# Optimization experiments

Hardware: AMD Instinct MI355X
Metric: run time of the kernel (lower is better)

Reference implementation:

```python
import jax, jax.numpy as jnp
import numpy as np

RESOLUTION = 256
THRESHOLD = 0.01
N_SAMPLES = 16_000_000


def setup_inputs() -> dict:
    key = jax.random.key(0)
    k1, k2 = jax.random.split(key)
    # torch.rand(n_samples, 3): uniform in [0,1) before AABB scaling
    points = jax.random.uniform(k1, (N_SAMPLES, 3), dtype=jnp.float32)
    # densities produced by the NeRF model; uniform [0,1) stand-in
    densities = jax.random.uniform(k2, (N_SAMPLES,), dtype=jnp.float32)
    return {"points": points, "densities": densities}


def reference(points, densities):
    aabb_min = jnp.array([-1.0, -1.0, -1.0], dtype=jnp.float32)
    aabb_max = jnp.array([1.0, 1.0, 1.0], dtype=jnp.float32)
    extent = aabb_max - aabb_min
    # scale unit-cube samples into the AABB (as update_grid does)
    pts = aabb_min + points * extent  # [N, 3]
    # voxel coords: ((p - min) / extent * R).long(), clamped to [0, R-1]
    coords = ((pts - aabb_min) / extent * RESOLUTION).astype(jnp.int32)
    coords = jnp.clip(coords, 0, RESOLUTION - 1)  # [N, 3]
    # loop writes 1.0 only where density > threshold; max over mask is equivalent
    occ = (densities > THRESHOLD).astype(jnp.float32)  # [N]
    grid = jnp.zeros((RESOLUTION, RESOLUTION, RESOLUTION), dtype=jnp.float32)
    grid = grid.at[coords[:, 0], coords[:, 1], coords[:, 2]].max(occ)
    return grid
```

## Files before the change

kernel.cpp:

```cpp
#include <hip/hip_runtime.h>

#define RES 256
#define THRESH 0.01f
#define GRID_VOX (RES * RES * RES)
#define NB 256
#define CHUNK_REC 8192
#define K1_BLOCKS 2048
#define QPT 8

typedef float vf4 __attribute__((ext_vector_type(4)));
typedef unsigned int u32;
typedef unsigned short u16;
typedef u32 vu4 __attribute__((ext_vector_type(4)));

__device__ __forceinline__ int voxel_coord(float p) {
    float a = -1.0f + p * 2.0f;
    float c = ((a + 1.0f) * 0.5f) * 256.0f;
    int v = (int)c;
    v = v < 0 ? 0 : v;
    v = v > (RES - 1) ? (RES - 1) : v;
    return v;
}

__global__ __launch_bounds__(256) void k1_bin256(const vf4* __restrict__ pts4,
                                                 const vf4* __restrict__ dens4,
                                                 u32* __restrict__ regions32,
                                                 u32* __restrict__ meta,
                                                 int n4) {
    __shared__ u32 s_cnt[NB];
    __shared__ u32 s_off[NB];
    __shared__ u32 s_buf[CHUNK_REC];

    const int tid  = threadIdx.x;
    const int lane = tid & 63;
    const int wid  = tid >> 6;
    const int T    = gridDim.x * blockDim.x;
    const int t0   = blockIdx.x * blockDim.x + tid;

    s_cnt[tid] = 0;
    __syncthreads();

    u32 rec[QPT * 4], rnk[QPT * 4], vbits = 0;

    #pragma unroll
    for (int h = 0; h < 2; ++h) {
        vf4 P[4][3], D[4];
        u32 qm = 0;
        #pragma unroll
        for (int s2 = 0; s2 < 4; ++s2) {
            int q = t0 + (h * 4 + s2) * T;
            if (q < n4) {
                qm |= 1u << s2;
                P[s2][0] = __builtin_nontemporal_load(&pts4[3 * q + 0]);
                P[s2][1] = __builtin_nontemporal_load(&pts4[3 * q + 1]);
                P[s2][2] = __builtin_nontemporal_load(&pts4[3 * q + 2]);
                D[s2]    = __builtin_nontemporal_load(&dens4[q]);
            }
        }
        #pragma unroll
        for (int s2 = 0; s2 < 4; ++s2) {
            if (!((qm >> s2) & 1u)) continue;
            float px[4] = {P[s2][0].x, P[s2][0].w, P[s2][1].z, P[s2][2].y};
            float py[4] = {P[s2][0].y, P[s2][1].x, P[s2][1].w, P[s2][2].z};
            float pz[4] = {P[s2][0].z, P[s2][1].y, P[s2][2].x, P[s2][2].w};
            float dd[4] = {D[s2].x, D[s2].y, D[s2].z, D[s2].w};
            #pragma unroll
            for (int k = 0; k < 4; ++k) {
                int kk = (h * 4 + s2) * 4 + k;
                u32 vox = ((u32)voxel_coord(px[k]) << 16) |
                          ((u32)voxel_coord(py[k]) << 8)  |
                           (u32)voxel_coord(pz[k]);
                rec[kk] = vox;
                if (dd[k] > THRESH) {
                    vbits |= 1u << kk;
                    rnk[kk] = atomicAdd(&s_cnt[vox >> 16], 1u);
                }
            }
        }
    }
    __syncthreads();

    if (wid == 0) {
        u32 c0 = s_cnt[4 * lane + 0], c1 = s_cnt[4 * lane + 1];
        u32 c2 = s_cnt[4 * lane + 2], c3 = s_cnt[4 * lane + 3];
        u32 w = c0 + c1 + c2 + c3;
        u32 x = w;
        #pragma unroll
        for (int dlt = 1; dlt < 64; dlt <<= 1) {
            u32 v = __shfl_up(x, dlt, 64);
            if (lane >= dlt) x += v;
        }
        u32 base = x - w;
        s_off[4 * lane + 0] = base;
        s_off[4 * lane + 1] = base + c0;
        s_off[4 * lane + 2] = base + c0 + c1;
        s_off[4 * lane + 3] = base + c0 + c1 + c2;
    }
    __syncthreads();

    const u32 c = blockIdx.x;

    meta[(size_t)c * NB + tid] = s_off[tid] | (s_cnt[tid] << 16);

    #pragma unroll
    for (int kk = 0; kk < QPT * 4; ++kk)
        if ((vbits >> kk) & 1u) {
            u32 b = rec[kk] >> 16;
            s_buf[s_off[b] + rnk[kk]] = rec[kk];
        }
    __syncthreads();

    u32 total = s_off[NB - 1] + s_cnt[NB - 1];
    u32 nw = (total + 1) >> 1;
    u32* reg = regions32 + (size_t)c * (CHUNK_REC / 2);
    for (u32 idx = tid; idx < nw; idx += 256u) {
        u32 lo = s_buf[2 * idx] & 0xFFFFu;
        u32 hi = s_buf[2 * idx + 1] & 0xFFFFu;
        reg[idx] = lo | (hi << 16);
    }
}

__global__ __launch_bounds__(1024) void k2_plane(const u16* __restrict__ regions16,
                                                 const u32* __restrict__ meta,
                                                 vf4* __restrict__ out4,
                                                 int nchunk) {
    extern __shared__ unsigned char plane[];
    const int ix  = blockIdx.x;
    const int tid = threadIdx.x;

    uint4* p16 = (uint4*)plane;
    #pragma unroll
    for (int j = 0; j < 4; ++j)
        p16[tid + j * 1024] = make_uint4(0u, 0u, 0u, 0u);
    __syncthreads();

    for (int c = tid; c < nchunk; c += 1024) {
        u32 m = meta[(size_t)c * NB + ix];
        u32 off = m & 0xFFFFu;
        u32 cnt = m >> 16;
        const u16* run = regions16 + (size_t)c * CHUNK_REC + off;
        for (u32 j = 0; j < cnt; ++j)
            plane[run[j]] = (unsigned char)1;
    }
    __syncthreads();

    const u32* pw = (const u32*)plane;
    vf4* dst = out4 + ((size_t)ix << 14);
    #pragma unroll
    for (int j = 0; j < 16; ++j) {
        int i = tid + j * 1024;
        u32 w = pw[i];
        vf4 f;
        f.x = (w & 0x000000FFu) ? 1.0f : 0.0f;
        f.y = (w & 0x0000FF00u) ? 1.0f : 0.0f;
        f.z = (w & 0x00FF0000u) ? 1.0f : 0.0f;
        f.w = (w & 0xFF000000u) ? 1.0f : 0.0f;
        __builtin_nontemporal_store(f, &dst[i]);
    }
}

__global__ void occ_scatter_bytes(const vf4* __restrict__ pts4,
                                  const vf4* __restrict__ dens4,
                                  unsigned char* __restrict__ bgrid, int n4) {
    int t = blockIdx.x * blockDim.x + threadIdx.x;
    int stride = gridDim.x * blockDim.x;
    for (int i = t; i < n4; i += stride) {
        vf4 p0 = __builtin_nontemporal_load(&pts4[3 * i + 0]);
        vf4 p1 = __builtin_nontemporal_load(&pts4[3 * i + 1]);
        vf4 p2 = __builtin_nontemporal_load(&pts4[3 * i + 2]);
        vf4 d  = __builtin_nontemporal_load(&dens4[i]);
        float px[4] = {p0.x, p0.w, p1.z, p2.y};
        float py[4] = {p0.y, p1.x, p1.w, p2.z};
        float pz[4] = {p0.z, p1.y, p2.x, p2.w};
        float dd[4] = {d.x, d.y, d.z, d.w};
        #pragma unroll
        for (int k = 0; k < 4; ++k) {
            if (dd[k] > THRESH) {
                int ix = voxel_coord(px[k]);
                int iy = voxel_coord(py[k]);
                int iz = voxel_coord(pz[k]);
                bgrid[((ix << 8) | iy) * RES + iz] = (unsigned char)1;
            }
        }
    }
}

__global__ void occ_expand(const uint4* __restrict__ bgrid16,
                           float4* __restrict__ grid4) {
    int i = blockIdx.x * blockDim.x + threadIdx.x;
    uint4 w = bgrid16[i];
    unsigned int ws[4] = {w.x, w.y, w.z, w.w};
    #pragma unroll
    for (int q = 0; q < 4; ++q) {
        unsigned int v = ws[q];
        float4 f;
        f.x = (v & 0x000000FFu) ? 1.0f : 0.0f;
        f.y = (v & 0x0000FF00u) ? 1.0f : 0.0f;
        f.z = (v & 0x00FF0000u) ? 1.0f : 0.0f;
        f.w = (v & 0xFF000000u) ? 1.0f : 0.0f;
        grid4[i * 4 + q] = f;
    }
}

__global__ void occ_scatter_float(const float4* __restrict__ pts4,
                                  const float4* __restrict__ dens4,
                                  float* __restrict__ grid, int n4) {
    int t = blockIdx.x * blockDim.x + threadIdx.x;
    int stride = gridDim.x * blockDim.x;
    for (int i = t; i < n4; i += stride) {
        float4 p0 = pts4[3 * i + 0];
        float4 p1 = pts4[3 * i + 1];
        float4 p2 = pts4[3 * i + 2];
        float4 d  = dens4[i];
        float px[4] = {p0.x, p0.w, p1.z, p2.y};
        float py[4] = {p0.y, p1.x, p1.w, p2.z};
        float pz[4] = {p0.z, p1.y, p2.x, p2.w};
        float dd[4] = {d.x, d.y, d.z, d.w};
        #pragma unroll
        for (int k = 0; k < 4; ++k) {
            if (dd[k] > THRESH) {
                int ix = voxel_coord(px[k]);
                int iy = voxel_coord(py[k]);
                int iz = voxel_coord(pz[k]);
                grid[((ix * RES) + iy) * RES + iz] = 1.0f;
            }
        }
    }
}

extern "C" void kernel_launch(void* const* d_in, const int* in_sizes, int n_in,
                              void* d_out, int out_size, void* d_ws, size_t ws_size,
                              hipStream_t stream) {
    const float* points    = (const float*)d_in[0];
    const float* densities = (const float*)d_in[1];
    float* grid = (float*)d_out;

    int n  = in_sizes[1];
    int n4 = n / 4;

    const int nchunk = K1_BLOCKS;

    size_t metaSize = (size_t)nchunk * NB * sizeof(u32);
    size_t need = metaSize + (size_t)nchunk * CHUNK_REC * sizeof(u16);

    bool covered = (size_t)K1_BLOCKS * 256 * QPT >= (size_t)n4;

    if (ws_size >= need && covered) {
        u32* meta      = (u32*)d_ws;
        u32* regions32 = (u32*)((char*)d_ws + metaSize);
        const u16* regions16 = (const u16*)regions32;

        k1_bin256<<<K1_BLOCKS, 256, 0, stream>>>(
            (const vf4*)points, (const vf4*)densities, regions32, meta, n4);

        k2_plane<<<NB, 1024, 65536, stream>>>(regions16, meta, (vf4*)grid, nchunk);
    } else if (ws_size >= (size_t)GRID_VOX) {
        unsigned char* bgrid = (unsigned char*)d_ws;
        (void)hipMemsetAsync(d_ws, 0, (size_t)GRID_VOX, stream);
        occ_scatter_bytes<<<2048, 256, 0, stream>>>(
            (const vf4*)points, (const vf4*)densities, bgrid, n4);
        occ_expand<<<GRID_VOX / (16 * 256), 256, 0, stream>>>(
            (const uint4*)bgrid, (float4*)grid);
    } else {
        (void)hipMemsetAsync(d_out, 0, (size_t)out_size * sizeof(float), stream);
        occ_scatter_float<<<2048, 256, 0, stream>>>(
            (const float4*)points, (const float4*)densities, grid, n4);
    }
}
```

Baseline: 107.4 us.

## Bin into 512 half-plane buckets and software-pipeline loads in binning kernel

The binning kernel now uses 512 buckets (half x-planes) instead of 256, so the plane kernel runs 512 blocks with 32KB LDS each, raising occupancy and parallelism in the scatter/expand stage. Loads are double-buffered in pairs with sched barriers to overlap memory with compute, and register rank arrays are replaced by a second atomic pass on per-bucket cursors. The LDS staging buffer is halved by writing 16-bit records directly, removing the repacking step. The cost is doubled metadata size, extra LDS atomics, and more meta reads in the plane kernel.

```diff
diff --git a/kernel.cpp b/kernel.cpp
--- a/kernel.cpp
+++ b/kernel.cpp
@@ -3,10 +3,10 @@
 #define RES 256
 #define THRESH 0.01f
 #define GRID_VOX (RES * RES * RES)
-#define NB 256
+#define NBUCK 512
 #define CHUNK_REC 8192
 #define K1_BLOCKS 2048
-#define QPT 8
+#define PAIRS 4
 
 typedef float vf4 __attribute__((ext_vector_type(4)));
 typedef unsigned int u32;
@@ -22,14 +22,16 @@
     return v;
 }
 
-__global__ __launch_bounds__(256) void k1_bin256(const vf4* __restrict__ pts4,
+__global__ __launch_bounds__(256) void k1_bin512(const vf4* __restrict__ pts4,
                                                  const vf4* __restrict__ dens4,
                                                  u32* __restrict__ regions32,
                                                  u32* __restrict__ meta,
                                                  int n4) {
-    __shared__ u32 s_cnt[NB];
-    __shared__ u32 s_off[NB];
-    __shared__ u32 s_buf[CHUNK_REC];
+    __shared__ u32 s_cnt[NBUCK];
+    __shared__ u32 s_off[NBUCK];
+    __shared__ u32 s_pos[NBUCK];
+    __shared__ u32 s_buf32[CHUNK_REC / 2];
+    u16* s_buf16 = (u16*)s_buf32;
 
     const int tid  = threadIdx.x;
     const int lane = tid & 63;
@@ -38,42 +40,64 @@
     const int t0   = blockIdx.x * blockDim.x + tid;
 
     s_cnt[tid] = 0;
-    __syncthreads();
-
-    u32 rec[QPT * 4], rnk[QPT * 4], vbits = 0;
-
-    #pragma unroll
-    for (int h = 0; h < 2; ++h) {
-        vf4 P[4][3], D[4];
-        u32 qm = 0;
-        #pragma unroll
-        for (int s2 = 0; s2 < 4; ++s2) {
-            int q = t0 + (h * 4 + s2) * T;
-            if (q < n4) {
-                qm |= 1u << s2;
-                P[s2][0] = __builtin_nontemporal_load(&pts4[3 * q + 0]);
-                P[s2][1] = __builtin_nontemporal_load(&pts4[3 * q + 1]);
-                P[s2][2] = __builtin_nontemporal_load(&pts4[3 * q + 2]);
-                D[s2]    = __builtin_nontemporal_load(&dens4[q]);
-            }
-        }
-        #pragma unroll
-        for (int s2 = 0; s2 < 4; ++s2) {
-            if (!((qm >> s2) & 1u)) continue;
-            float px[4] = {P[s2][0].x, P[s2][0].w, P[s2][1].z, P[s2][2].y};
-            float py[4] = {P[s2][0].y, P[s2][1].x, P[s2][1].w, P[s2][2].z};
-            float pz[4] = {P[s2][0].z, P[s2][1].y, P[s2][2].x, P[s2][2].w};
-            float dd[4] = {D[s2].x, D[s2].y, D[s2].z, D[s2].w};
+    s_cnt[tid + 256] = 0;
+    __syncthreads();
+
+    u32 rec[PAIRS * 8];
+    u32 vbits = 0;
+
+    vf4 P[2][2][3], D[2][2];
+    u32 qm[2];
+
+    qm[0] = 0;
+    #pragma unroll
+    for (int j = 0; j < 2; ++j) {
+        int q = t0 + j * T;
+        if (q < n4) {
+            qm[0] |= 1u << j;
+            P[0][j][0] = __builtin_nontemporal_load(&pts4[3 * q + 0]);
+            P[0][j][1] = __builtin_nontemporal_load(&pts4[3 * q + 1]);
+            P[0][j][2] = __builtin_nontemporal_load(&pts4[3 * q + 2]);
+            D[0][j]    = __builtin_nontemporal_load(&dens4[q]);
+        }
+    }
+    __builtin_amdgcn_sched_barrier(0);
+
+    #pragma unroll
+    for (int p = 0; p < PAIRS; ++p) {
+        const int cur = p & 1, nxt = cur ^ 1;
+        if (p < PAIRS - 1) {
+            qm[nxt] = 0;
+            #pragma unroll
+            for (int j = 0; j < 2; ++j) {
+                int q = t0 + ((p + 1) * 2 + j) * T;
+                if (q < n4) {
+                    qm[nxt] |= 1u << j;
+                    P[nxt][j][0] = __builtin_nontemporal_load(&pts4[3 * q + 0]);
+                    P[nxt][j][1] = __builtin_nontemporal_load(&pts4[3 * q + 1]);
+                    P[nxt][j][2] = __builtin_nontemporal_load(&pts4[3 * q + 2]);
+                    D[nxt][j]    = __builtin_nontemporal_load(&dens4[q]);
+                }
+            }
+            __builtin_amdgcn_sched_barrier(0);
+        }
+        #pragma unroll
+        for (int j = 0; j < 2; ++j) {
+            if (!((qm[cur] >> j) & 1u)) continue;
+            float px[4] = {P[cur][j][0].x, P[cur][j][0].w, P[cur][j][1].z, P[cur][j][2].y};
+            float py[4] = {P[cur][j][0].y, P[cur][j][1].x, P[cur][j][1].w, P[cur][j][2].z};
+            float pz[4] = {P[cur][j][0].z, P[cur][j][1].y, P[cur][j][2].x, P[cur][j][2].w};
+            float dd[4] = {D[cur][j].x, D[cur][j].y, D[cur][j].z, D[cur][j].w};
             #pragma unroll
             for (int k = 0; k < 4; ++k) {
-                int kk = (h * 4 + s2) * 4 + k;
+                int kk = p * 8 + j * 4 + k;
                 u32 vox = ((u32)voxel_coord(px[k]) << 16) |
                           ((u32)voxel_coord(py[k]) << 8)  |
                            (u32)voxel_coord(pz[k]);
                 rec[kk] = vox;
                 if (dd[k] > THRESH) {
                     vbits |= 1u << kk;
-                    rnk[kk] = atomicAdd(&s_cnt[vox >> 16], 1u);
+                    atomicAdd(&s_cnt[vox >> 15], 1u);
                 }
             }
         }
@@ -81,9 +105,9 @@
     __syncthreads();
 
     if (wid == 0) {
-        u32 c0 = s_cnt[4 * lane + 0], c1 = s_cnt[4 * lane + 1];
-        u32 c2 = s_cnt[4 * lane + 2], c3 = s_cnt[4 * lane + 3];
-        u32 w = c0 + c1 + c2 + c3;
+        u32 cc[8], w = 0;
+        #pragma unroll
+        for (int e = 0; e < 8; ++e) { cc[e] = s_cnt[8 * lane + e]; w += cc[e]; }
         u32 x = w;
         #pragma unroll
         for (int dlt = 1; dlt < 64; dlt <<= 1) {
@@ -91,33 +115,33 @@
             if (lane >= dlt) x += v;
         }
         u32 base = x - w;
-        s_off[4 * lane + 0] = base;
-        s_off[4 * lane + 1] = base + c0;
-        s_off[4 * lane + 2] = base + c0 + c1;
-        s_off[4 * lane + 3] = base + c0 + c1 + c2;
+        #pragma unroll
+        for (int e = 0; e < 8; ++e) {
+            s_off[8 * lane + e] = base;
+            s_pos[8 * lane + e] = base;
+            base += cc[e];
+        }
     }
     __syncthreads();
 
     const u32 c = blockIdx.x;
 
-    meta[(size_t)c * NB + tid] = s_off[tid] | (s_cnt[tid] << 16);
-
-    #pragma unroll
-    for (int kk = 0; kk < QPT * 4; ++kk)
+    meta[(size_t)c * NBUCK + tid]       = s_off[tid]       | (s_cnt[tid] << 16);
+    meta[(size_t)c * NBUCK + tid + 256] = s_off[tid + 256] | (s_cnt[tid + 256] << 16);
+
+    #pragma unroll
+    for (int kk = 0; kk < PAIRS * 8; ++kk)
         if ((vbits >> kk) & 1u) {
-            u32 b = rec[kk] >> 16;
-            s_buf[s_off[b] + rnk[kk]] = rec[kk];
-        }
-    __syncthreads();
-
-    u32 total = s_off[NB - 1] + s_cnt[NB - 1];
+            u32 pos = atomicAdd(&s_pos[rec[kk] >> 15], 1u);
+            s_buf16[pos] = (u16)rec[kk];
+        }
+    __syncthreads();
+
+    u32 total = s_off[NBUCK - 1] + s_cnt[NBUCK - 1];
     u32 nw = (total + 1) >> 1;
     u32* reg = regions32 + (size_t)c * (CHUNK_REC / 2);
-    for (u32 idx = tid; idx < nw; idx += 256u) {
-        u32 lo = s_buf[2 * idx] & 0xFFFFu;
-        u32 hi = s_buf[2 * idx + 1] & 0xFFFFu;
-        reg[idx] = lo | (hi << 16);
-    }
+    for (u32 idx = tid; idx < nw; idx += 256u)
+        reg[idx] = s_buf32[idx];
 }
 
 __global__ __launch_bounds__(1024) void k2_plane(const u16* __restrict__ regions16,
@@ -125,29 +149,29 @@
                                                  vf4* __restrict__ out4,
                                                  int nchunk) {
     extern __shared__ unsigned char plane[];
-    const int ix  = blockIdx.x;
+    const int bid = blockIdx.x;
     const int tid = threadIdx.x;
 
     uint4* p16 = (uint4*)plane;
     #pragma unroll
-    for (int j = 0; j < 4; ++j)
+    for (int j = 0; j < 2; ++j)
         p16[tid + j * 1024] = make_uint4(0u, 0u, 0u, 0u);
     __syncthreads();
 
     for (int c = tid; c < nchunk; c += 1024) {
-        u32 m = meta[(size_t)c * NB + ix];
+        u32 m = meta[(size_t)c * NBUCK + bid];
         u32 off = m & 0xFFFFu;
         u32 cnt = m >> 16;
         const u16* run = regions16 + (size_t)c * CHUNK_REC + off;
         for (u32 j = 0; j < cnt; ++j)
-            plane[run[j]] = (unsigned char)1;
+            plane[run[j] & 0x7FFFu] = (unsigned char)1;
     }
     __syncthreads();
 
     const u32* pw = (const u32*)plane;
-    vf4* dst = out4 + ((size_t)ix << 14);
-    #pragma unroll
-    for (int j = 0; j < 16; ++j) {
+    vf4* dst = out4 + ((size_t)bid << 13);
+    #pragma unroll
+    for (int j = 0; j < 8; ++j) {
         int i = tid + j * 1024;
         u32 w = pw[i];
         vf4 f;
@@ -240,20 +264,20 @@
 
     const int nchunk = K1_BLOCKS;
 
-    size_t metaSize = (size_t)nchunk * NB * sizeof(u32);
+    size_t metaSize = (size_t)nchunk * NBUCK * sizeof(u32);
     size_t need = metaSize + (size_t)nchunk * CHUNK_REC * sizeof(u16);
 
-    bool covered = (size_t)K1_BLOCKS * 256 * QPT >= (size_t)n4;
+    bool covered = (size_t)K1_BLOCKS * 256 * (PAIRS * 2) >= (size_t)n4;
 
     if (ws_size >= need && covered) {
         u32* meta      = (u32*)d_ws;
         u32* regions32 = (u32*)((char*)d_ws + metaSize);
         const u16* regions16 = (const u16*)regions32;
 
-        k1_bin256<<<K1_BLOCKS, 256, 0, stream>>>(
+        k1_bin512<<<K1_BLOCKS, 256, 0, stream>>>(
             (const vf4*)points, (const vf4*)densities, regions32, meta, n4);
 
-        k2_plane<<<NB, 1024, 65536, stream>>>(regions16, meta, (vf4*)grid, nchunk);
+        k2_plane<<<2 * RES, 1024, 32768, stream>>>(regions16, meta, (vf4*)grid, nchunk);
     } else if (ws_size >= (size_t)GRID_VOX) {
         unsigned char* bgrid = (unsigned char*)d_ws;
         (void)hipMemsetAsync(d_ws, 0, (size_t)GRID_VOX, stream);
```

New measurement: 146.8 us. +36.8%, slower.

## Store 16-bit records in LDS with vector copy-out; wave-per-chunk scatter in plane kernel

Applied to the files above, without the earlier changes.

The binning kernel now writes 16-bit voxel indices straight into a half-size shared buffer and copies the region out to global memory with 16-byte vector stores, replacing the 32-bit staging and pack loop. The plane kernel now gives each chunk to a whole wavefront, whose lanes read the run together and set bytes in parallel, instead of one thread walking each run serially. The aim is less LDS traffic and fewer global store instructions in k1, and coalesced reads with better load balance in k2. Copy-out now rounds up to multiples of 8 records, so a few unused entries get written past the valid count.

```diff
diff --git a/kernel.cpp b/kernel.cpp
--- a/kernel.cpp
+++ b/kernel.cpp
@@ -24,12 +24,13 @@
 
 __global__ __launch_bounds__(256) void k1_bin256(const vf4* __restrict__ pts4,
                                                  const vf4* __restrict__ dens4,
-                                                 u32* __restrict__ regions32,
+                                                 vu4* __restrict__ regions4,
                                                  u32* __restrict__ meta,
                                                  int n4) {
     __shared__ u32 s_cnt[NB];
     __shared__ u32 s_off[NB];
-    __shared__ u32 s_buf[CHUNK_REC];
+    __shared__ u32 s_buf32[CHUNK_REC / 2];
+    u16* s_buf16 = (u16*)s_buf32;
 
     const int tid  = threadIdx.x;
     const int lane = tid & 63;
@@ -104,20 +105,16 @@
 
     #pragma unroll
     for (int kk = 0; kk < QPT * 4; ++kk)
-        if ((vbits >> kk) & 1u) {
-            u32 b = rec[kk] >> 16;
-            s_buf[s_off[b] + rnk[kk]] = rec[kk];
-        }
+        if ((vbits >> kk) & 1u)
+            s_buf16[s_off[rec[kk] >> 16] + rnk[kk]] = (u16)rec[kk];
     __syncthreads();
 
     u32 total = s_off[NB - 1] + s_cnt[NB - 1];
-    u32 nw = (total + 1) >> 1;
-    u32* reg = regions32 + (size_t)c * (CHUNK_REC / 2);
-    for (u32 idx = tid; idx < nw; idx += 256u) {
-        u32 lo = s_buf[2 * idx] & 0xFFFFu;
-        u32 hi = s_buf[2 * idx + 1] & 0xFFFFu;
-        reg[idx] = lo | (hi << 16);
-    }
+    u32 n16 = (total + 7) >> 3;
+    vu4* reg = regions4 + (size_t)c * (CHUNK_REC / 8);
+    const vu4* sb4 = (const vu4*)s_buf32;
+    for (u32 idx = tid; idx < n16; idx += 256u)
+        reg[idx] = sb4[idx];
 }
 
 __global__ __launch_bounds__(1024) void k2_plane(const u16* __restrict__ regions16,
@@ -125,8 +122,10 @@
                                                  vf4* __restrict__ out4,
                                                  int nchunk) {
     extern __shared__ unsigned char plane[];
-    const int ix  = blockIdx.x;
-    const int tid = threadIdx.x;
+    const int ix   = blockIdx.x;
+    const int tid  = threadIdx.x;
+    const int lane = tid & 63;
+    const int wid  = tid >> 6;
 
     uint4* p16 = (uint4*)plane;
     #pragma unroll
@@ -134,12 +133,12 @@
         p16[tid + j * 1024] = make_uint4(0u, 0u, 0u, 0u);
     __syncthreads();
 
-    for (int c = tid; c < nchunk; c += 1024) {
+    for (int c = wid; c < nchunk; c += 16) {
         u32 m = meta[(size_t)c * NB + ix];
         u32 off = m & 0xFFFFu;
         u32 cnt = m >> 16;
         const u16* run = regions16 + (size_t)c * CHUNK_REC + off;
-        for (u32 j = 0; j < cnt; ++j)
+        for (u32 j = lane; j < cnt; j += 64u)
             plane[run[j]] = (unsigned char)1;
     }
     __syncthreads();
@@ -246,12 +245,12 @@
     bool covered = (size_t)K1_BLOCKS * 256 * QPT >= (size_t)n4;
 
     if (ws_size >= need && covered) {
-        u32* meta      = (u32*)d_ws;
-        u32* regions32 = (u32*)((char*)d_ws + metaSize);
-        const u16* regions16 = (const u16*)regions32;
+        u32* meta     = (u32*)d_ws;
+        vu4* regions4 = (vu4*)((char*)d_ws + metaSize);
+        const u16* regions16 = (const u16*)regions4;
 
         k1_bin256<<<K1_BLOCKS, 256, 0, stream>>>(
-            (const vf4*)points, (const vf4*)densities, regions32, meta, n4);
+            (const vf4*)points, (const vf4*)densities, regions4, meta, n4);
 
         k2_plane<<<NB, 1024, 65536, stream>>>(regions16, meta, (vf4*)grid, nchunk);
     } else if (ws_size >= (size_t)GRID_VOX) {
```

After: 159.1 us. 48.2% more time.
